# Optimization experiments

Hardware: AMD Instinct MI355X
Metric: run time of the kernel (lower is better)

Reference implementation:

```python
import jax, jax.numpy as jnp
import numpy as np

IN_DIM = 512
CMP_DIM = 512
OUT_DIM = 512
BOARD = (8, 8, 8, 8)
BATCH = 4


def setup_inputs() -> dict:
    key = jax.random.key(0)
    ks = jax.random.split(key, 9)
    shape = (BATCH,) + BOARD + (IN_DIM,)
    query_X = jax.random.normal(ks[0], shape, dtype=jnp.float32)
    key_X = jax.random.normal(ks[1], shape, dtype=jnp.float32)
    value_X = jax.random.normal(ks[2], shape, dtype=jnp.float32)
    s = 1.0 / np.sqrt(IN_DIM)
    W_Q = jax.random.uniform(ks[3], (IN_DIM, CMP_DIM), jnp.float32, -s, s)
    b_Q = jax.random.uniform(ks[4], (CMP_DIM,), jnp.float32, -s, s)
    W_K = jax.random.uniform(ks[5], (IN_DIM, CMP_DIM), jnp.float32, -s, s)
    b_K = jax.random.uniform(ks[6], (CMP_DIM,), jnp.float32, -s, s)
    W_V = jax.random.uniform(ks[7], (IN_DIM, OUT_DIM), jnp.float32, -s, s)
    b_V = jax.random.uniform(ks[8], (OUT_DIM,), jnp.float32, -s, s)
    return {"query_X": query_X, "key_X": key_X, "value_X": value_X,
            "W_Q": W_Q, "b_Q": b_Q, "W_K": W_K, "b_K": b_K, "W_V": W_V, "b_V": b_V}


def reference(query_X, key_X, value_X, W_Q, b_Q, W_K, b_K, W_V, b_V):
    B = query_X.shape[0]
    # project then flatten board dims: (B, N, d)
    q = (query_X @ W_Q + b_Q).reshape(B, -1, CMP_DIM)
    k = (key_X @ W_K + b_K).reshape(B, -1, CMP_DIM)
    v = (value_X @ W_V + b_V).reshape(B, -1, OUT_DIM)
    scores = jnp.einsum('bqc,bkc->bqk', q, k) / jnp.sqrt(jnp.float32(CMP_DIM))
    att = jax.nn.softmax(scores, axis=-1)
    return jnp.einsum('bqk,bkd->bqd', att, v)
```

## Files before the change

kernel.cpp:

```cpp
#include <hip/hip_runtime.h>
#include <hip/hip_bf16.h>
#include <stdint.h>


typedef __attribute__((ext_vector_type(8))) short short8;
typedef __attribute__((ext_vector_type(4))) short short4v;
typedef __attribute__((ext_vector_type(4))) float f32x4;

#define SCALE_L2E 0.06375880243f
#define FIXED_M   12.0f

__device__ __forceinline__ short f2bf(float f) {
    union { float f; uint32_t u; } v; v.f = f;
    uint32_t r = (v.u + 0x7fffu + ((v.u >> 16) & 1u)) >> 16;
    return (short)r;
}

__device__ __forceinline__ f32x4 mfma16x16x32(short8 a, short8 b, f32x4 c) {
    return __builtin_amdgcn_mfma_f32_16x16x32_bf16(a, b, c, 0, 0, 0);
}

#define GLOAD_LDS16(gp, lp)                                                      \
    __builtin_amdgcn_global_load_lds(                                            \
        (const __attribute__((address_space(1))) uint32_t*)(gp),                 \
        (__attribute__((address_space(3))) uint32_t*)(lp), 16, 0, 0)

__global__ __launch_bounds__(256) void prep_wt(
        const float* __restrict__ wq, const float* __restrict__ wk,
        const float* __restrict__ wv,
        short* __restrict__ wqt, short* __restrict__ wkt, short* __restrict__ wvt) {
    __shared__ float tile[32][33];
    const float* src = blockIdx.z == 0 ? wq : (blockIdx.z == 1 ? wk : wv);
    short*       dst = blockIdx.z == 0 ? wqt : (blockIdx.z == 1 ? wkt : wvt);
    int tx = threadIdx.x, ty = threadIdx.y;
    int n0 = blockIdx.x * 32, k0 = blockIdx.y * 32;
#pragma unroll
    for (int j = 0; j < 32; j += 8)
        tile[ty + j][tx] = src[(size_t)(k0 + ty + j) * 512 + n0 + tx];
    __syncthreads();
#pragma unroll
    for (int j = 0; j < 32; j += 8)
        dst[(size_t)(n0 + ty + j) * 512 + k0 + tx] = f2bf(tile[tx][ty + j]);
}

__device__ __forceinline__ void proj_body(
        const float* __restrict__ Xf, const short* __restrict__ WT,
        const float* __restrict__ bias, short* __restrict__ out, int transpose_v,
        short* sA, short* sB, short* sT) {
    const int tid = threadIdx.x;
    const int w = tid >> 6, lane = tid & 63;
    const int l15 = lane & 15, quad = lane >> 4;
    const int wr = w >> 1, wc = w & 1;
    const int m0 = blockIdx.x * 128;
    const int n0 = blockIdx.y * 128;

    f32x4 acc[4][4];
#pragma unroll
    for (int i = 0; i < 4; ++i)
#pragma unroll
        for (int j = 0; j < 4; ++j) acc[i][j] = f32x4{0.f, 0.f, 0.f, 0.f};

    for (int k0 = 0; k0 < 512; k0 += 64) {
        __syncthreads();
        float4 av[4][2];
#pragma unroll
        for (int p = 0; p < 4; ++p) {
            int i = p * 256 + tid;
            int row = i >> 3, cl = i & 7;
            const float4* src = (const float4*)(Xf + (size_t)(m0 + row) * 512 + k0 + cl * 8);
            av[p][0] = src[0];
            av[p][1] = src[1];
        }
#pragma unroll
        for (int p = 0; p < 4; ++p) {
            int i = p * 256 + tid;
            int row = i >> 3, cl = i & 7, cg = cl ^ (row & 7);
            GLOAD_LDS16(WT + (size_t)(n0 + row) * 512 + k0 + cg * 8,
                        sB + (size_t)(i & ~63) * 8);
        }
#pragma unroll
        for (int p = 0; p < 4; ++p) {
            int i = p * 256 + tid;
            int row = i >> 3, cl = i & 7, cg = cl ^ (row & 7);
            uint32_t u0, u1, u2, u3;
            asm("v_cvt_pk_bf16_f32 %0, %1, %2" : "=v"(u0) : "v"(av[p][0].x), "v"(av[p][0].y));
            asm("v_cvt_pk_bf16_f32 %0, %1, %2" : "=v"(u1) : "v"(av[p][0].z), "v"(av[p][0].w));
            asm("v_cvt_pk_bf16_f32 %0, %1, %2" : "=v"(u2) : "v"(av[p][1].x), "v"(av[p][1].y));
            asm("v_cvt_pk_bf16_f32 %0, %1, %2" : "=v"(u3) : "v"(av[p][1].z), "v"(av[p][1].w));
            short8 s;
            ((uint32_t*)&s)[0] = u0; ((uint32_t*)&s)[1] = u1;
            ((uint32_t*)&s)[2] = u2; ((uint32_t*)&s)[3] = u3;
            *(short8*)&sA[(size_t)(row * 8 + cg) * 8] = s;
        }
        __syncthreads();
#pragma unroll
        for (int ks = 0; ks < 2; ++ks) {
            short8 af[4], bfr[4];
#pragma unroll
            for (int mt = 0; mt < 4; ++mt) {
                int row = wr * 64 + mt * 16 + l15;
                int c = (ks * 4 + quad) ^ (row & 7);
                af[mt] = *(const short8*)&sA[(row * 8 + c) * 8];
            }
#pragma unroll
            for (int nt = 0; nt < 4; ++nt) {
                int row = wc * 64 + nt * 16 + l15;
                int c = (ks * 4 + quad) ^ (row & 7);
                bfr[nt] = *(const short8*)&sB[(row * 8 + c) * 8];
            }
#pragma unroll
            for (int mt = 0; mt < 4; ++mt)
#pragma unroll
                for (int nt = 0; nt < 4; ++nt)
                    acc[mt][nt] = mfma16x16x32(af[mt], bfr[nt], acc[mt][nt]);
        }
    }
    if (!transpose_v) {
#pragma unroll
        for (int nt = 0; nt < 4; ++nt) {
            float bv = bias[n0 + wc * 64 + nt * 16 + l15];
#pragma unroll
            for (int mt = 0; mt < 4; ++mt)
#pragma unroll
                for (int r = 0; r < 4; ++r) {
                    int gm = m0 + wr * 64 + mt * 16 + quad * 4 + r;
                    int gn = n0 + wc * 64 + nt * 16 + l15;
                    out[(size_t)gm * 512 + gn] = f2bf(acc[mt][nt][r] + bv);
                }
        }
    } else {
        __syncthreads();
#pragma unroll
        for (int nt = 0; nt < 4; ++nt) {
            float bv = bias[n0 + wc * 64 + nt * 16 + l15];
            int dl = wc * 64 + nt * 16 + l15;
#pragma unroll
            for (int mt = 0; mt < 4; ++mt) {
                int pl = wr * 64 + mt * 16 + quad * 4;
                short4v s;
                s.x = f2bf(acc[mt][nt][0] + bv);
                s.y = f2bf(acc[mt][nt][1] + bv);
                s.z = f2bf(acc[mt][nt][2] + bv);
                s.w = f2bf(acc[mt][nt][3] + bv);
                *(short4v*)&sT[dl * 136 + pl] = s;
            }
        }
        __syncthreads();
        const int b = m0 >> 12, posb = m0 & 4095;
        const int col = (tid & 15) * 8;
#pragma unroll
        for (int rnd = 0; rnd < 8; ++rnd) {
            int dl = rnd * 16 + (tid >> 4);
            *(short8*)&out[((size_t)b * 512 + n0 + dl) * 4096 + posb + col] =
                *(const short8*)&sT[dl * 136 + col];
        }
    }
}

__global__ __launch_bounds__(256) void proj3(
        const float* __restrict__ qX, const float* __restrict__ kX,
        const float* __restrict__ vX,
        const short* __restrict__ wqt, const short* __restrict__ wkt,
        const short* __restrict__ wvt,
        const float* __restrict__ bQ, const float* __restrict__ bK,
        const float* __restrict__ bV,
        short* __restrict__ oq, short* __restrict__ ok, short* __restrict__ ovt) {
    __shared__ __align__(16) short smem[128 * 136];
    const int z = blockIdx.z;
    proj_body(z == 0 ? qX : (z == 1 ? kX : vX),
              z == 0 ? wqt : (z == 1 ? wkt : wvt),
              z == 0 ? bQ : (z == 1 ? bK : bV),
              z == 0 ? oq : (z == 1 ? ok : ovt), z == 2 ? 1 : 0,
              smem, smem + 8192, smem);
}

__global__ __launch_bounds__(512, 2) void flash_attn(
        const short* __restrict__ qb, const short* __restrict__ kb,
        const short* __restrict__ vtb, float* __restrict__ out) {
    __shared__ __align__(16) short sK[64 * 64 * 8];
    __shared__ __align__(16) short sV[512 * 8 * 8];
    __shared__ __align__(16) short sP[64 * 72];
    __shared__ __align__(16) float sL[64 * 4];

    const int tid = threadIdx.x;
    const int w = tid >> 6, lane = tid & 63;
    const int l15 = lane & 15, quad = lane >> 4;
    const int qg = w >> 2, kg = w & 3;

    const int n = blockIdx.x + (blockIdx.y << 6);
    const int batch = (n >> 1) & 3;
    const int q0 = ((((n >> 3) << 1) | (n & 1))) << 6;

    const short* qbase = qb  + (size_t)batch * 4096 * 512;
    const short* kbase = kb  + (size_t)batch * 4096 * 512;
    const short* vbase = vtb + (size_t)batch * 512 * 4096;

    const int key0 = tid >> 6;
    const int kcg  = (tid & 63) ^ (key0 & 7);
    const short* ksrc0 = kbase + (size_t)key0 * 512 + kcg * 8;
    const int kdst0 = (tid & ~63) * 8;
    const int d0  = tid >> 3;
    const int vcg = (tid & 7) ^ (d0 & 7);
    const short* vsrc0 = vbase + (size_t)d0 * 4096 + vcg * 8;
    const int vdst0 = (tid & ~63) * 8;

    short8 qf[2][16];
#pragma unroll
    for (int qmt = 0; qmt < 2; ++qmt) {
        const short* qrow = qbase + (size_t)(q0 + qg * 32 + qmt * 16 + l15) * 512 + quad * 8;
#pragma unroll
        for (int ks = 0; ks < 16; ++ks)
            qf[qmt][ks] = *(const short8*)(qrow + ks * 32);
    }

    f32x4 acc[4][4];
#pragma unroll
    for (int i = 0; i < 4; ++i)
#pragma unroll
        for (int j = 0; j < 4; ++j) acc[i][j] = f32x4{0.f, 0.f, 0.f, 0.f};
    float lp[2][4] = {{0.f, 0.f, 0.f, 0.f}, {0.f, 0.f, 0.f, 0.f}};

#pragma unroll
    for (int it = 0; it < 8; ++it)
        GLOAD_LDS16(ksrc0 + it * 4096, sK + kdst0 + it * 4096);
    __syncthreads();

    for (int t = 0; t < 64; ++t) {
        const int t0 = t * 64;

        {
            const short* vp = vsrc0 + t0;
#pragma unroll
            for (int it = 0; it < 8; ++it)
                GLOAD_LDS16(vp + (size_t)it * 262144, sV + vdst0 + it * 4096);
        }
        __builtin_amdgcn_sched_barrier(0);

        f32x4 s0 = f32x4{0.f, 0.f, 0.f, 0.f};
        f32x4 s1 = f32x4{0.f, 0.f, 0.f, 0.f};
        const int key = kg * 16 + l15;
        const int ksw = key & 7;
#pragma unroll
        for (int ks = 0; ks < 16; ++ks) {
            short8 kf = *(const short8*)&sK[(key * 64 + ((ks * 4 + quad) ^ ksw)) * 8];
            s0 = mfma16x16x32(qf[0][ks], kf, s0);
            s1 = mfma16x16x32(qf[1][ks], kf, s1);
        }
#pragma unroll
        for (int qmt = 0; qmt < 2; ++qmt) {
            f32x4 sv = qmt ? s1 : s0;
#pragma unroll
            for (int r = 0; r < 4; ++r) {
                float p = __builtin_amdgcn_exp2f(
                    __builtin_fmaf(sv[r], SCALE_L2E, -FIXED_M));
                lp[qmt][r] += p;
                sP[(qg * 32 + qmt * 16 + quad * 4 + r) * 72 + kg * 16 + l15] = f2bf(p);
            }
        }

        __syncthreads();

        if (t < 63) {
            const short* kp = ksrc0 + (size_t)(t0 + 64) * 512;
#pragma unroll
            for (int it = 0; it < 8; ++it)
                GLOAD_LDS16(kp + it * 4096, sK + kdst0 + it * 4096);
        }
        __builtin_amdgcn_sched_barrier(0);

#pragma unroll
        for (int kc = 0; kc < 2; ++kc) {
            short8 pa[4], vf[4];
#pragma unroll
            for (int mt = 0; mt < 4; ++mt)
                pa[mt] = *(const short8*)&sP[(mt * 16 + l15) * 72 + kc * 32 + quad * 8];
#pragma unroll
            for (int nt = 0; nt < 4; ++nt) {
                int d = w * 64 + nt * 16 + l15;
                vf[nt] = *(const short8*)&sV[(d * 8 + ((kc * 4 + quad) ^ (d & 7))) * 8];
            }
#pragma unroll
            for (int mt = 0; mt < 4; ++mt)
#pragma unroll
                for (int nt = 0; nt < 4; ++nt)
                    acc[mt][nt] = mfma16x16x32(pa[mt], vf[nt], acc[mt][nt]);
        }

        __syncthreads();
    }
#pragma unroll
    for (int qmt = 0; qmt < 2; ++qmt)
#pragma unroll
        for (int r = 0; r < 4; ++r) {
            float v = lp[qmt][r];
            v += __shfl_xor(v, 1);
            v += __shfl_xor(v, 2);
            v += __shfl_xor(v, 4);
            v += __shfl_xor(v, 8);
            if (l15 == 0)
                sL[(qg * 32 + qmt * 16 + quad * 4 + r) * 4 + kg] = v;
        }
    __syncthreads();
#pragma unroll
    for (int mt = 0; mt < 4; ++mt)
#pragma unroll
        for (int r = 0; r < 4; ++r) {
            int row = mt * 16 + quad * 4 + r;
            float linv = 1.0f / (sL[row * 4] + sL[row * 4 + 1] +
                                 sL[row * 4 + 2] + sL[row * 4 + 3]);
            float* orow = out + ((size_t)batch * 4096 + q0 + row) * 512 + w * 64 + l15;
#pragma unroll
            for (int nt = 0; nt < 4; ++nt)
                orow[nt * 16] = acc[mt][nt][r] * linv;
        }
}

extern "C" void kernel_launch(void* const* d_in, const int* in_sizes, int n_in,
                              void* d_out, int out_size, void* d_ws, size_t ws_size,
                              hipStream_t stream) {
    const float* qX = (const float*)d_in[0];
    const float* kX = (const float*)d_in[1];
    const float* vX = (const float*)d_in[2];
    const float* WQ = (const float*)d_in[3];
    const float* bQ = (const float*)d_in[4];
    const float* WK = (const float*)d_in[5];
    const float* bK = (const float*)d_in[6];
    const float* WV = (const float*)d_in[7];
    const float* bV = (const float*)d_in[8];
    float* out = (float*)d_out;

    short* qb  = (short*)d_ws;
    short* kb  = qb  + (size_t)16384 * 512;
    short* vtb = kb  + (size_t)16384 * 512;
    short* wqt = vtb + (size_t)16384 * 512;
    short* wkt = wqt + (size_t)512 * 512;
    short* wvt = wkt + (size_t)512 * 512;

    prep_wt<<<dim3(16, 16, 3), dim3(32, 8), 0, stream>>>(WQ, WK, WV, wqt, wkt, wvt);
    proj3<<<dim3(128, 4, 3), 256, 0, stream>>>(qX, kX, vX, wqt, wkt, wvt,
                                               bQ, bK, bV, qb, kb, vtb);
    flash_attn<<<dim3(64, 4), 512, 0, stream>>>(qb, kb, vtb, out);
}
```

Before: 340.7 us.

## Double-buffer projection GEMM K-loop, swizzle block order, drop LDS transpose for V

The projection GEMM now double-buffers its A and B tiles in LDS. It prefetches the next W tile through global_load_lds and the next X tile into registers while the MFMAs run on the current buffer, which cuts one barrier per K step. Blocks are remapped from a 1D grid so that groups of 8 M tiles share the 4 N tiles, which is meant to improve L2 reuse of X. The transposed V output now writes 4-element strips straight to global memory instead of staging through LDS. This saves barriers but gives narrower, less coalesced stores, and the doubled LDS and registers may lower occupancy.

Result: no change. 340.9 us (+0.1%).

```diff
diff --git a/kernel.cpp b/kernel.cpp
--- a/kernel.cpp
+++ b/kernel.cpp
@@ -46,13 +46,14 @@
 __device__ __forceinline__ void proj_body(
         const float* __restrict__ Xf, const short* __restrict__ WT,
         const float* __restrict__ bias, short* __restrict__ out, int transpose_v,
-        short* sA, short* sB, short* sT) {
+        short* sm) {
     const int tid = threadIdx.x;
     const int w = tid >> 6, lane = tid & 63;
     const int l15 = lane & 15, quad = lane >> 4;
     const int wr = w >> 1, wc = w & 1;
-    const int m0 = blockIdx.x * 128;
-    const int n0 = blockIdx.y * 128;
+    const int id = blockIdx.x;
+    const int m0 = ((id & 7) | ((id >> 5) << 3)) * 128;
+    const int n0 = ((id >> 3) & 3) * 128;
 
     f32x4 acc[4][4];
 #pragma unroll
@@ -60,39 +61,65 @@
 #pragma unroll
         for (int j = 0; j < 4; ++j) acc[i][j] = f32x4{0.f, 0.f, 0.f, 0.f};
 
-    for (int k0 = 0; k0 < 512; k0 += 64) {
-        __syncthreads();
-        float4 av[4][2];
-#pragma unroll
-        for (int p = 0; p < 4; ++p) {
-            int i = p * 256 + tid;
-            int row = i >> 3, cl = i & 7;
-            const float4* src = (const float4*)(Xf + (size_t)(m0 + row) * 512 + k0 + cl * 8);
-            av[p][0] = src[0];
-            av[p][1] = src[1];
-        }
-#pragma unroll
-        for (int p = 0; p < 4; ++p) {
-            int i = p * 256 + tid;
-            int row = i >> 3, cl = i & 7, cg = cl ^ (row & 7);
-            GLOAD_LDS16(WT + (size_t)(n0 + row) * 512 + k0 + cg * 8,
-                        sB + (size_t)(i & ~63) * 8);
-        }
-#pragma unroll
-        for (int p = 0; p < 4; ++p) {
-            int i = p * 256 + tid;
-            int row = i >> 3, cl = i & 7, cg = cl ^ (row & 7);
-            uint32_t u0, u1, u2, u3;
-            asm("v_cvt_pk_bf16_f32 %0, %1, %2" : "=v"(u0) : "v"(av[p][0].x), "v"(av[p][0].y));
-            asm("v_cvt_pk_bf16_f32 %0, %1, %2" : "=v"(u1) : "v"(av[p][0].z), "v"(av[p][0].w));
-            asm("v_cvt_pk_bf16_f32 %0, %1, %2" : "=v"(u2) : "v"(av[p][1].x), "v"(av[p][1].y));
-            asm("v_cvt_pk_bf16_f32 %0, %1, %2" : "=v"(u3) : "v"(av[p][1].z), "v"(av[p][1].w));
-            short8 s;
-            ((uint32_t*)&s)[0] = u0; ((uint32_t*)&s)[1] = u1;
-            ((uint32_t*)&s)[2] = u2; ((uint32_t*)&s)[3] = u3;
-            *(short8*)&sA[(size_t)(row * 8 + cg) * 8] = s;
-        }
-        __syncthreads();
+    float4 av[2][4][2];
+
+#define LOADA(B, K0)                                                             \
+    _Pragma("unroll")                                                            \
+    for (int p = 0; p < 4; ++p) {                                                \
+        int i = p * 256 + tid;                                                   \
+        int row = i >> 3, cl = i & 7;                                            \
+        const float4* s =                                                        \
+            (const float4*)(Xf + (size_t)(m0 + row) * 512 + (K0) + cl * 8);      \
+        av[B][p][0] = s[0];                                                      \
+        av[B][p][1] = s[1];                                                      \
+    }
+
+#define STAGEB(DST, K0)                                                          \
+    _Pragma("unroll")                                                            \
+    for (int p = 0; p < 4; ++p) {                                                \
+        int i = p * 256 + tid;                                                   \
+        int row = i >> 3, cl = i & 7, cg = cl ^ (row & 7);                       \
+        GLOAD_LDS16(WT + (size_t)(n0 + row) * 512 + (K0) + cg * 8,               \
+                    (DST) + (size_t)(i & ~63) * 8);                              \
+    }
+
+#define CVTA(DST, B)                                                             \
+    _Pragma("unroll")                                                            \
+    for (int p = 0; p < 4; ++p) {                                                \
+        int i = p * 256 + tid;                                                   \
+        int row = i >> 3, cl = i & 7, cg = cl ^ (row & 7);                       \
+        uint32_t u0, u1, u2, u3;                                                 \
+        asm("v_cvt_pk_bf16_f32 %0, %1, %2" : "=v"(u0)                            \
+            : "v"(av[B][p][0].x), "v"(av[B][p][0].y));                           \
+        asm("v_cvt_pk_bf16_f32 %0, %1, %2" : "=v"(u1)                            \
+            : "v"(av[B][p][0].z), "v"(av[B][p][0].w));                           \
+        asm("v_cvt_pk_bf16_f32 %0, %1, %2" : "=v"(u2)                            \
+            : "v"(av[B][p][1].x), "v"(av[B][p][1].y));                           \
+        asm("v_cvt_pk_bf16_f32 %0, %1, %2" : "=v"(u3)                            \
+            : "v"(av[B][p][1].z), "v"(av[B][p][1].w));                           \
+        short8 sv8;                                                              \
+        ((uint32_t*)&sv8)[0] = u0; ((uint32_t*)&sv8)[1] = u1;                    \
+        ((uint32_t*)&sv8)[2] = u2; ((uint32_t*)&sv8)[3] = u3;                    \
+        *(short8*)&(DST)[(size_t)(row * 8 + cg) * 8] = sv8;                      \
+    }
+
+    LOADA(0, 0)
+    STAGEB(sm + 8192, 0)
+    CVTA(sm, 0)
+    LOADA(1, 64)
+    __syncthreads();
+
+#pragma unroll
+    for (int kk = 0; kk < 8; ++kk) {
+        const int cur = kk & 1, nxt = cur ^ 1;
+        short* sAc = sm + cur * 16384;
+        short* sBc = sAc + 8192;
+        short* sAn = sm + nxt * 16384;
+        short* sBn = sAn + 8192;
+
+        if (kk < 7) STAGEB(sBn, (kk + 1) * 64)
+        if (kk < 6) LOADA(cur, (kk + 2) * 64)
+
 #pragma unroll
         for (int ks = 0; ks < 2; ++ks) {
             short8 af[4], bfr[4];
@@ -100,13 +127,13 @@
             for (int mt = 0; mt < 4; ++mt) {
                 int row = wr * 64 + mt * 16 + l15;
                 int c = (ks * 4 + quad) ^ (row & 7);
-                af[mt] = *(const short8*)&sA[(row * 8 + c) * 8];
+                af[mt] = *(const short8*)&sAc[(row * 8 + c) * 8];
             }
 #pragma unroll
             for (int nt = 0; nt < 4; ++nt) {
                 int row = wc * 64 + nt * 16 + l15;
                 int c = (ks * 4 + quad) ^ (row & 7);
-                bfr[nt] = *(const short8*)&sB[(row * 8 + c) * 8];
+                bfr[nt] = *(const short8*)&sBc[(row * 8 + c) * 8];
             }
 #pragma unroll
             for (int mt = 0; mt < 4; ++mt)
@@ -114,7 +141,15 @@
                 for (int nt = 0; nt < 4; ++nt)
                     acc[mt][nt] = mfma16x16x32(af[mt], bfr[nt], acc[mt][nt]);
         }
-    }
+
+        if (kk < 7) CVTA(sAn, nxt)
+
+        __syncthreads();
+    }
+#undef LOADA
+#undef STAGEB
+#undef CVTA
+
     if (!transpose_v) {
 #pragma unroll
         for (int nt = 0; nt < 4; ++nt) {
@@ -129,30 +164,21 @@
                 }
         }
     } else {
-        __syncthreads();
 #pragma unroll
         for (int nt = 0; nt < 4; ++nt) {
             float bv = bias[n0 + wc * 64 + nt * 16 + l15];
-            int dl = wc * 64 + nt * 16 + l15;
+            int gn = n0 + wc * 64 + nt * 16 + l15;
 #pragma unroll
             for (int mt = 0; mt < 4; ++mt) {
-                int pl = wr * 64 + mt * 16 + quad * 4;
+                int gm = m0 + wr * 64 + mt * 16 + quad * 4;
+                int b = gm >> 12, pos = gm & 4095;
                 short4v s;
                 s.x = f2bf(acc[mt][nt][0] + bv);
                 s.y = f2bf(acc[mt][nt][1] + bv);
                 s.z = f2bf(acc[mt][nt][2] + bv);
                 s.w = f2bf(acc[mt][nt][3] + bv);
-                *(short4v*)&sT[dl * 136 + pl] = s;
-            }
-        }
-        __syncthreads();
-        const int b = m0 >> 12, posb = m0 & 4095;
-        const int col = (tid & 15) * 8;
-#pragma unroll
-        for (int rnd = 0; rnd < 8; ++rnd) {
-            int dl = rnd * 16 + (tid >> 4);
-            *(short8*)&out[((size_t)b * 512 + n0 + dl) * 4096 + posb + col] =
-                *(const short8*)&sT[dl * 136 + col];
+                *(short4v*)&out[((size_t)b * 512 + gn) * 4096 + pos] = s;
+            }
         }
     }
 }
@@ -165,13 +191,13 @@
         const float* __restrict__ bQ, const float* __restrict__ bK,
         const float* __restrict__ bV,
         short* __restrict__ oq, short* __restrict__ ok, short* __restrict__ ovt) {
-    __shared__ __align__(16) short smem[128 * 136];
+    __shared__ __align__(16) short smem[2 * 16384];
     const int z = blockIdx.z;
     proj_body(z == 0 ? qX : (z == 1 ? kX : vX),
               z == 0 ? wqt : (z == 1 ? wkt : wvt),
               z == 0 ? bQ : (z == 1 ? bK : bV),
               z == 0 ? oq : (z == 1 ? ok : ovt), z == 2 ? 1 : 0,
-              smem, smem + 8192, smem);
+              smem);
 }
 
 __global__ __launch_bounds__(512, 2) void flash_attn(
@@ -337,7 +363,7 @@
     short* wvt = wkt + (size_t)512 * 512;
 
     prep_wt<<<dim3(16, 16, 3), dim3(32, 8), 0, stream>>>(WQ, WK, WV, wqt, wkt, wvt);
-    proj3<<<dim3(128, 4, 3), 256, 0, stream>>>(qX, kX, vX, wqt, wkt, wvt,
+    proj3<<<dim3(512, 1, 3), 256, 0, stream>>>(qX, kX, vX, wqt, wkt, wvt,
                                                bQ, bK, bV, qb, kb, vtb);
     flash_attn<<<dim3(64, 4), 512, 0, stream>>>(qb, kb, vtb, out);
 }
```
